# Kernel optimization log

Hardware: AMD Instinct MI355X
Metric: run time of the kernel (lower is better)

The kernel has to match this reference:

```python
import jax, jax.numpy as jnp
import numpy as np

NUM_GROUPS = 64  # matches fill_max of ids; all groups present w.h.p. so unique-inverse == ids


def setup_inputs() -> dict:
    key = jax.random.key(0)
    ks = jax.random.split(key, 8)
    B, N, D = 8, 8192, 512
    s = 1.0 / np.sqrt(D)
    return {
        "x": jax.random.normal(ks[0], (B, N, D), dtype=jnp.float32),
        "ids": jax.random.randint(ks[1], (N,), 0, NUM_GROUPS),
        "w1": jax.random.normal(ks[2], (D, D), dtype=jnp.float32) * s,
        "b1": jax.random.normal(ks[3], (D,), dtype=jnp.float32) * s,
        "w2": jax.random.normal(ks[4], (D, D), dtype=jnp.float32) * s,
        "b2": jax.random.normal(ks[5], (D,), dtype=jnp.float32) * s,
        "w3": jax.random.normal(ks[6], (D, D), dtype=jnp.float32) * s,
        "b3": jax.random.normal(ks[7], (D,), dtype=jnp.float32) * s,
    }


def reference(x, ids, w1, b1, w2, b2, w3, b3):
    # x: [B, N, D]; ids: [N] group labels in [0, NUM_GROUPS)
    G = NUM_GROUPS
    a = jnp.einsum('bnd,ed->bne', x, w1) + b1          # linear1 logits
    v = jnp.einsum('bnd,ed->bne', x, w2) + b2          # linear2 values
    # move segment axis to front: [N, B, D]
    aT = jnp.transpose(a, (1, 0, 2))
    vT = jnp.transpose(v, (1, 0, 2))
    # per-group stable softmax along the segment axis
    mx = jax.lax.stop_gradient(jax.ops.segment_max(aT, ids, num_segments=G))  # [G,B,D]
    ex = jnp.exp(aT - mx[ids])
    denom = jax.ops.segment_sum(ex, ids, num_segments=G)                      # [G,B,D]
    wts = ex / denom[ids]                                                     # [N,B,D]
    # weighted scatter-sum of values -> [G, B, D] -> [B, G, D]
    y = jnp.transpose(jax.ops.segment_sum(vT * wts, ids, num_segments=G), (1, 0, 2))
    out = jnp.einsum('bgd,ed->bge', y, w3) + b3        # linear3
    # expand: gather group outputs back to per-element rows -> [B, N, D]
    return out[:, ids]
```

## Files before the change

kernel.cpp:

```cpp
#include <hip/hip_runtime.h>
#include <hip/hip_bf16.h>
#include <math.h>

#define B_ 8
#define N_ 8192
#define D_ 512
#define G_ 64
#define M_ (B_ * N_)

typedef short bf16x8 __attribute__((ext_vector_type(8)));
typedef float f32x4 __attribute__((ext_vector_type(4)));

__device__ __forceinline__ unsigned short f2bf(float f) {
    __hip_bfloat16 h = __float2bfloat16(f);
    return *reinterpret_cast<unsigned short*>(&h);
}
__device__ __forceinline__ void gload_lds16(const void* g, void* l) {
    __builtin_amdgcn_global_load_lds((const __attribute__((address_space(1))) void*)g,
                                     (__attribute__((address_space(3))) void*)l,
                                     16, 0, 0);
}

__global__ __launch_bounds__(256) void cast_xp(const float* __restrict__ x,
                                               const int* __restrict__ perm,
                                               unsigned short* __restrict__ xb) {
    const int total = M_ * 128;
    for (int idx = blockIdx.x * 256 + threadIdx.x; idx < total;
         idx += gridDim.x * 256) {
        const int row = idx >> 7;
        const int q = (idx & 127) * 4;
        const int b = row >> 13;
        const int i = row & 8191;
        const float* src = x + (((size_t)(b << 13) + perm[i]) << 9) + q;
        float4 f = *(const float4*)src;
        ushort4 u;
        u.x = f2bf(f.x); u.y = f2bf(f.y); u.z = f2bf(f.z); u.w = f2bf(f.w);
        *(ushort4*)(xb + ((size_t)row << 9) + q) = u;
    }
}

__global__ __launch_bounds__(256) void cast_w(const float* __restrict__ w1,
                                              const float* __restrict__ b1,
                                              const float* __restrict__ w2,
                                              const float* __restrict__ b2,
                                              unsigned short* __restrict__ wB,
                                              float* __restrict__ biasB) {
    int t = blockIdx.x * 256 + threadIdx.x;
    int idx = t * 4;
    int row = idx >> 9;
    int col = idx & 511;
    const float* src = (row < 512) ? (w1 + (size_t)row * 512 + col)
                                   : (w2 + (size_t)(row - 512) * 512 + col);
    float4 f = *(const float4*)src;
    ushort4 u;
    u.x = f2bf(f.x); u.y = f2bf(f.y); u.z = f2bf(f.z); u.w = f2bf(f.w);
    *(ushort4*)(wB + idx) = u;
    if (t < 1024) biasB[t] = (t < 512) ? b1[t] : b2[t - 512];
}

__global__ __launch_bounds__(256) void bl_hist(const int* __restrict__ ids,
                                               int* __restrict__ counts,
                                               int* __restrict__ stripbase) {
    __shared__ int sid[N_];
    __shared__ int sc[256];
    const int g = blockIdx.x;
    const int t = threadIdx.x;
    for (int i = t; i < N_; i += 256) sid[i] = ids[i];
    __syncthreads();
    int c = 0;
    const int nb = t * 32;
#pragma unroll 8
    for (int k = 0; k < 32; ++k) c += (sid[nb + k] == g) ? 1 : 0;
    sc[t] = c;
    __syncthreads();
    if (t == 0) {
        int run = 0;
        for (int i = 0; i < 256; ++i) { int v = sc[i]; sc[i] = run; run += v; }
        counts[g] = run;
    }
    __syncthreads();
    stripbase[g * 256 + t] = sc[t];
}

__global__ __launch_bounds__(256) void bl_emit(const int* __restrict__ ids,
                                               const int* __restrict__ counts,
                                               const int* __restrict__ stripbase,
                                               int* __restrict__ baseO,
                                               int* __restrict__ fgO,
                                               int* __restrict__ perm) {
    __shared__ int sid[N_];
    __shared__ int sb[G_ + 1];
    __shared__ int sbs;
    const int g = blockIdx.x;
    const int t = threadIdx.x;
    for (int i = t; i < N_; i += 256) sid[i] = ids[i];
    if (t == 0) {
        int a = 0;
        for (int gg = 0; gg < G_; ++gg) { sb[gg] = a; a += counts[gg]; }
        sb[G_] = a;
        sbs = sb[g];
    }
    __syncthreads();
    if (g == 0 && t < G_) {
        baseO[t] = sb[t];
        const int row = t * 128;
        int gg = 0;
        while (gg + 1 < G_ && sb[gg + 1] <= row) ++gg;
        fgO[t] = gg;
    }
    int pos = sbs + stripbase[g * 256 + t];
    const int nb = t * 32;
    for (int k = 0; k < 32; ++k)
        if (sid[nb + k] == g) perm[pos++] = nb + k;
}

__global__ __launch_bounds__(512, 2) void gemm_fused(const unsigned short* __restrict__ xb,
                                                     const unsigned short* __restrict__ wB,
                                                     const float* __restrict__ biasB,
                                                     const int* __restrict__ base,
                                                     const int* __restrict__ fg,
                                                     float* __restrict__ pt) {
    extern __shared__ unsigned short smem[];
    unsigned short* lsA = smem;
    unsigned short* lsB = smem + 32768;

    const int o  = blockIdx.x;
    const int mt = (o & 7) + ((o >> 5) << 3);
    const int nt = (o >> 3) & 3;
    const int b  = mt >> 5;
    const int tlb = (mt & 31) * 2;
    const int c0 = nt * 128;

    const int tid = threadIdx.x;
    const int l = tid & 63;
    const int w = tid >> 6;
    const int wm = w >> 2;
    const int wn = w & 3;
    const int lr = l >> 3;
    const int lslot = l & 7;
    const int fr = l & 15;
    const int kq = l >> 4;
    const int scol = 8 * (lslot ^ lr);

    f32x4 acc[8][4];
#pragma unroll
    for (int i = 0; i < 8; ++i)
#pragma unroll
        for (int j = 0; j < 4; ++j) acc[i][j] = (f32x4){0.f, 0.f, 0.f, 0.f};

    const size_t abase = (((size_t)b << 13) + (size_t)(mt & 31) * 256) << 9;

    auto stage8 = [&](int slot, int kt) {
#pragma unroll
        for (int q = 0; q < 4; ++q) {
            const int c = w * 4 + q;
            const int row = c * 8 + lr;
            gload_lds16(xb + abase + ((size_t)row << 9) + kt + scol,
                        lsA + slot * 16384 + c * 512);
        }
#pragma unroll
        for (int q = 0; q < 4; ++q) {
            const int c = w * 4 + q;
            const int srcrow = ((c >> 2) & 1) * 512 + c0 + (c >> 3) * 32
                             + (c & 3) * 8 + lr;
            gload_lds16(wB + ((size_t)srcrow << 9) + kt + scol,
                        lsB + slot * 16384 + c * 512);
        }
    };

    stage8(0, 0);
    stage8(1, 64);

    for (int i4 = 0; i4 < 4; ++i4) {
#pragma unroll
        for (int half = 0; half < 2; ++half) {
            const int slot = half;
            const bool doStage = (half == 0) ? (i4 > 0) : (i4 < 3);
            if (doStage) stage8(1 - half, (2 * i4 + 1 + half) * 64);
            if (doStage || (half == 0)) {
                asm volatile("s_waitcnt vmcnt(8)" ::: "memory");
            } else {
                asm volatile("s_waitcnt vmcnt(0)" ::: "memory");
            }
            __builtin_amdgcn_s_barrier();

            const unsigned short* pA = lsA + slot * 16384;
            const unsigned short* pB = lsB + slot * 16384;
            bf16x8 bq[4];
#pragma unroll
            for (int ks = 0; ks < 2; ++ks) {
                const int ib = 8 * ((ks * 4 + kq) ^ (fr & 7));
#pragma unroll
                for (int ih = 0; ih < 2; ++ih) {
                    bf16x8 a[4];
#pragma unroll
                    for (int i = 0; i < 4; ++i)
                        a[i] = *(const bf16x8*)&pA[(wm * 128 + (ih * 4 + i) * 16 + fr) * 64 + ib];
                    if (ih == 0) {
#pragma unroll
                        for (int j = 0; j < 4; ++j)
                            bq[j] = *(const bf16x8*)&pB[(wn * 64 + j * 16 + fr) * 64 + ib];
                    }
                    __builtin_amdgcn_s_barrier();
                    __builtin_amdgcn_s_setprio(1);
#pragma unroll
                    for (int i = 0; i < 4; ++i)
#pragma unroll
                        for (int j = 0; j < 4; ++j)
                            acc[ih * 4 + i][j] = __builtin_amdgcn_mfma_f32_16x16x32_bf16(
                                a[i], bq[j], acc[ih * 4 + i][j], 0, 0, 0);
                    __builtin_amdgcn_s_setprio(0);
                    __builtin_amdgcn_s_barrier();
                }
            }
        }
    }

    const int tl = tlb + wm;
    const int fg0 = fg[tl];
    const int bnd0 = (fg0 + 1 < G_) ? base[fg0 + 1] : (1 << 30);
    const int bnd1 = (fg0 + 2 < G_) ? base[fg0 + 2] : (1 << 30);
    const int bnd2 = (fg0 + 3 < G_) ? base[fg0 + 3] : (1 << 30);
    float b1c[2], b2c[2];
#pragma unroll
    for (int j = 0; j < 2; ++j) {
        const int col = c0 + wn * 32 + j * 16 + fr;
        b1c[j] = biasB[col];
        b2c[j] = biasB[512 + col];
    }
    float dp[4][2] = {}, yp[4][2] = {};
    const int rbase = tl * 128 + kq * 4;
#pragma unroll
    for (int i = 0; i < 8; ++i)
#pragma unroll
        for (int rr = 0; rr < 4; ++rr) {
            const int row = rbase + i * 16 + rr;
            const int s = (row >= bnd0) + (row >= bnd1) + (row >= bnd2);
#pragma unroll
            for (int j = 0; j < 2; ++j) {
                const float e = __expf(acc[i][j][rr] + b1c[j]);
                const float ey = e * (acc[i][j + 2][rr] + b2c[j]);
#pragma unroll
                for (int s2 = 0; s2 < 4; ++s2) {
                    dp[s2][j] += (s == s2) ? e : 0.f;
                    yp[s2][j] += (s == s2) ? ey : 0.f;
                }
            }
        }
#pragma unroll
    for (int s2 = 0; s2 < 4; ++s2)
#pragma unroll
        for (int j = 0; j < 2; ++j) {
            dp[s2][j] += __shfl_xor(dp[s2][j], 16);
            dp[s2][j] += __shfl_xor(dp[s2][j], 32);
            yp[s2][j] += __shfl_xor(yp[s2][j], 16);
            yp[s2][j] += __shfl_xor(yp[s2][j], 32);
        }
    if (kq == 0) {
#pragma unroll
        for (int s2 = 0; s2 < 4; ++s2)
#pragma unroll
            for (int j = 0; j < 2; ++j) {
                const int colp = c0 + wn * 32 + j * 16 + fr;
                float2 v = make_float2(dp[s2][j], yp[s2][j]);
                *(float2*)&pt[(((size_t)(b * 64 + tl) * 4 + s2) * 512 + colp) * 2] = v;
            }
    }
}

__global__ __launch_bounds__(256) void combineC(const float* __restrict__ pt,
                                                const int* __restrict__ base,
                                                const int* __restrict__ counts,
                                                const int* __restrict__ fg,
                                                float* __restrict__ y) {
    const int g = blockIdx.x, b = blockIdx.y;
    const int bs = base[g];
    int cnt = counts[g];
    if (cnt == 0) cnt = 1;
    const int t0 = bs >> 7, t1 = (bs + cnt - 1) >> 7;
    for (int c = threadIdx.x; c < 512; c += 256) {
        float d = 0.f, yy = 0.f;
        for (int t = t0; t <= t1; ++t) {
            const int s = g - fg[t];
            if (s >= 0 && s < 4) {
                const float* p = &pt[((((size_t)(b * 64 + t)) * 4 + s) * 512 + c) * 2];
                d += p[0];
                yy += p[1];
            }
        }
        y[((size_t)(b * G_ + g)) * 512 + c] = yy / d;
    }
}

__global__ __launch_bounds__(256) void gemm3(const float* __restrict__ y,
                                             const float* __restrict__ w3,
                                             const float* __restrict__ b3,
                                             float* __restrict__ out_small) {
    __shared__ float ys[16][68];
    __shared__ float wss[16][68];
    const int m0 = blockIdx.x * 64;
    const int n0 = blockIdx.y * 64;
    const int tid = threadIdx.x;
    const int tr = tid >> 4;
    const int tc = tid & 15;
    const int lrow = tid >> 2;
    const int lk4 = (tid & 3) * 4;

    float acc[4][4] = {};

    for (int k0 = 0; k0 < D_; k0 += 16) {
        float4 yv = *(const float4*)(y + (size_t)(m0 + lrow) * D_ + k0 + lk4);
        float4 wv = *(const float4*)(w3 + (size_t)(n0 + lrow) * D_ + k0 + lk4);
        __syncthreads();
        ys[lk4 + 0][lrow] = yv.x;  ys[lk4 + 1][lrow] = yv.y;
        ys[lk4 + 2][lrow] = yv.z;  ys[lk4 + 3][lrow] = yv.w;
        wss[lk4 + 0][lrow] = wv.x; wss[lk4 + 1][lrow] = wv.y;
        wss[lk4 + 2][lrow] = wv.z; wss[lk4 + 3][lrow] = wv.w;
        __syncthreads();
#pragma unroll
        for (int kk = 0; kk < 16; ++kk) {
            float4 y4 = *(const float4*)&ys[kk][tr * 4];
            float4 w4 = *(const float4*)&wss[kk][tc * 4];
            float ya[4] = {y4.x, y4.y, y4.z, y4.w};
            float wa[4] = {w4.x, w4.y, w4.z, w4.w};
#pragma unroll
            for (int i = 0; i < 4; ++i)
#pragma unroll
                for (int j = 0; j < 4; ++j)
                    acc[i][j] = fmaf(ya[i], wa[j], acc[i][j]);
        }
    }

    float bb[4];
#pragma unroll
    for (int j = 0; j < 4; ++j) bb[j] = b3[n0 + tc * 4 + j];
#pragma unroll
    for (int i = 0; i < 4; ++i) {
        size_t o = (size_t)(m0 + tr * 4 + i) * D_ + n0 + tc * 4;
        float4 r;
        r.x = acc[i][0] + bb[0]; r.y = acc[i][1] + bb[1];
        r.z = acc[i][2] + bb[2]; r.w = acc[i][3] + bb[3];
        *(float4*)(out_small + o) = r;
    }
}

__global__ __launch_bounds__(256) void gather_out(const int* __restrict__ ids,
                                                  const float* __restrict__ out_small,
                                                  float* __restrict__ out) {
    const int c = blockIdx.x * 256 + threadIdx.x;
    const int per_row = D_ / 4;
    const int b = c / (N_ * per_row);
    const int rem = c % (N_ * per_row);
    const int n = rem / per_row;
    const int q = rem % per_row;
    const int g = ids[n];
    float4 val = *(const float4*)(out_small + ((size_t)b * G_ + g) * D_ + q * 4);
    *(float4*)(out + (size_t)c * 4) = val;
}

extern "C" void kernel_launch(void* const* d_in, const int* in_sizes, int n_in,
                              void* d_out, int out_size, void* d_ws, size_t ws_size,
                              hipStream_t stream) {
    (void)in_sizes; (void)n_in; (void)out_size; (void)ws_size;
    const float* x   = (const float*)d_in[0];
    const int*   ids = (const int*)d_in[1];
    const float* w1  = (const float*)d_in[2];
    const float* b1  = (const float*)d_in[3];
    const float* w2  = (const float*)d_in[4];
    const float* b2  = (const float*)d_in[5];
    const float* w3  = (const float*)d_in[6];
    const float* b3  = (const float*)d_in[7];
    float* out = (float*)d_out;

    float* ws_f = (float*)d_ws;
    unsigned short* xb = (unsigned short*)ws_f;
    float* after_xb  = ws_f + 16777216;
    unsigned short* wB = (unsigned short*)after_xb;
    float* biasB     = after_xb + 262144;
    float* pt        = biasB + 1024;
    float* y         = pt + 2097152;
    float* out_small = y + 262144;
    int*   perm      = (int*)(out_small + 262144);
    int*   base      = perm + N_;
    int*   counts    = base + G_;
    int*   fg        = counts + G_;
    int*   stripbase = fg + G_;

    hipFuncSetAttribute((const void*)gemm_fused,
                        hipFuncAttributeMaxDynamicSharedMemorySize, 131072);

    hipLaunchKernelGGL(bl_hist, dim3(G_), dim3(256), 0, stream, ids, counts, stripbase);
    hipLaunchKernelGGL(bl_emit, dim3(G_), dim3(256), 0, stream,
                       ids, counts, stripbase, base, fg, perm);
    hipLaunchKernelGGL(cast_w, dim3(512), dim3(256), 0, stream, w1, b1, w2, b2, wB, biasB);
    hipLaunchKernelGGL(cast_xp, dim3(2048), dim3(256), 0, stream, x, perm, xb);
    hipLaunchKernelGGL(gemm_fused, dim3(1024), dim3(512), 131072, stream,
                       xb, wB, biasB, base, fg, pt);
    hipLaunchKernelGGL(combineC, dim3(G_, B_), dim3(256), 0, stream, pt, base, counts, fg, y);
    hipLaunchKernelGGL(gemm3, dim3(8, 8), dim3(256), 0, stream, y, w3, b3, out_small);
    hipLaunchKernelGGL(gather_out, dim3(32768), dim3(256), 0, stream, ids, out_small, out);
}
```

Before: 204.6 us.

## Interleave next-tile global-to-LDS prefetch across MFMA phases in GEMM main loop

```diff
diff --git a/kernel.cpp b/kernel.cpp
--- a/kernel.cpp
+++ b/kernel.cpp
@@ -150,68 +150,66 @@
 
     const size_t abase = (((size_t)b << 13) + (size_t)(mt & 31) * 256) << 9;
 
-    auto stage8 = [&](int slot, int kt) {
-#pragma unroll
-        for (int q = 0; q < 4; ++q) {
-            const int c = w * 4 + q;
-            const int row = c * 8 + lr;
-            gload_lds16(xb + abase + ((size_t)row << 9) + kt + scol,
-                        lsA + slot * 16384 + c * 512);
-        }
-#pragma unroll
-        for (int q = 0; q < 4; ++q) {
-            const int c = w * 4 + q;
-            const int srcrow = ((c >> 2) & 1) * 512 + c0 + (c >> 3) * 32
-                             + (c & 3) * 8 + lr;
-            gload_lds16(wB + ((size_t)srcrow << 9) + kt + scol,
-                        lsB + slot * 16384 + c * 512);
-        }
+    auto stageA = [&](int slot, int kt, int q) {
+        const int c = w * 4 + q;
+        const int row = c * 8 + lr;
+        gload_lds16(xb + abase + ((size_t)row << 9) + kt + scol,
+                    lsA + slot * 16384 + c * 512);
     };
-
-    stage8(0, 0);
-    stage8(1, 64);
-
-    for (int i4 = 0; i4 < 4; ++i4) {
-#pragma unroll
-        for (int half = 0; half < 2; ++half) {
-            const int slot = half;
-            const bool doStage = (half == 0) ? (i4 > 0) : (i4 < 3);
-            if (doStage) stage8(1 - half, (2 * i4 + 1 + half) * 64);
-            if (doStage || (half == 0)) {
-                asm volatile("s_waitcnt vmcnt(8)" ::: "memory");
-            } else {
-                asm volatile("s_waitcnt vmcnt(0)" ::: "memory");
-            }
-            __builtin_amdgcn_s_barrier();
-
-            const unsigned short* pA = lsA + slot * 16384;
-            const unsigned short* pB = lsB + slot * 16384;
-            bf16x8 bq[4];
-#pragma unroll
-            for (int ks = 0; ks < 2; ++ks) {
-                const int ib = 8 * ((ks * 4 + kq) ^ (fr & 7));
-#pragma unroll
-                for (int ih = 0; ih < 2; ++ih) {
-                    bf16x8 a[4];
-#pragma unroll
-                    for (int i = 0; i < 4; ++i)
-                        a[i] = *(const bf16x8*)&pA[(wm * 128 + (ih * 4 + i) * 16 + fr) * 64 + ib];
-                    if (ih == 0) {
-#pragma unroll
-                        for (int j = 0; j < 4; ++j)
-                            bq[j] = *(const bf16x8*)&pB[(wn * 64 + j * 16 + fr) * 64 + ib];
-                    }
-                    __builtin_amdgcn_s_barrier();
-                    __builtin_amdgcn_s_setprio(1);
-#pragma unroll
-                    for (int i = 0; i < 4; ++i)
-#pragma unroll
-                        for (int j = 0; j < 4; ++j)
-                            acc[ih * 4 + i][j] = __builtin_amdgcn_mfma_f32_16x16x32_bf16(
-                                a[i], bq[j], acc[ih * 4 + i][j], 0, 0, 0);
-                    __builtin_amdgcn_s_setprio(0);
-                    __builtin_amdgcn_s_barrier();
+    auto stageB = [&](int slot, int kt, int q) {
+        const int c = w * 4 + q;
+        const int srcrow = ((c >> 2) & 1) * 512 + c0 + (c >> 3) * 32
+                         + (c & 3) * 8 + lr;
+        gload_lds16(wB + ((size_t)srcrow << 9) + kt + scol,
+                    lsB + slot * 16384 + c * 512);
+    };
+
+#pragma unroll
+    for (int q = 0; q < 4; ++q) stageA(0, 0, q);
+#pragma unroll
+    for (int q = 0; q < 4; ++q) stageB(0, 0, q);
+    asm volatile("s_waitcnt vmcnt(0)" ::: "memory");
+    __builtin_amdgcn_s_barrier();
+
+    for (int t = 0; t < 8; ++t) {
+        const int slot = t & 1;
+        const int so = slot ^ 1;
+        const int kn = (t + 1) * 64;
+        const bool pf = (t < 7);
+        const unsigned short* pA = lsA + slot * 16384;
+        const unsigned short* pB = lsB + slot * 16384;
+        bf16x8 a[4], bq[4];
+
+#pragma unroll
+        for (int ks = 0; ks < 2; ++ks) {
+            const int ib = 8 * ((ks * 4 + kq) ^ (fr & 7));
+#pragma unroll
+            for (int ih = 0; ih < 2; ++ih) {
+                if (pf) {
+                    if (ks == 0 && ih == 0) { stageA(so, kn, 0); stageA(so, kn, 1); stageB(so, kn, 0); }
+                    else if (ks == 0 && ih == 1) { stageA(so, kn, 2); stageA(so, kn, 3); stageB(so, kn, 1); }
+                    else if (ks == 1 && ih == 0) { stageB(so, kn, 2); stageB(so, kn, 3); }
                 }
+#pragma unroll
+                for (int i = 0; i < 4; ++i)
+                    a[i] = *(const bf16x8*)&pA[(wm * 128 + (ih * 4 + i) * 16 + fr) * 64 + ib];
+                if (ih == 0) {
+#pragma unroll
+                    for (int j = 0; j < 4; ++j)
+                        bq[j] = *(const bf16x8*)&pB[(wn * 64 + j * 16 + fr) * 64 + ib];
+                }
+                __builtin_amdgcn_s_barrier();
+                __builtin_amdgcn_s_setprio(1);
+#pragma unroll
+                for (int i = 0; i < 4; ++i)
+#pragma unroll
+                    for (int j = 0; j < 4; ++j)
+                        acc[ih * 4 + i][j] = __builtin_amdgcn_mfma_f32_16x16x32_bf16(
+                            a[i], bq[j], acc[ih * 4 + i][j], 0, 0, 0);
+                __builtin_amdgcn_s_setprio(0);
+                if (ks == 1 && ih == 1)
+                    asm volatile("s_waitcnt vmcnt(0)" ::: "memory");
+                __builtin_amdgcn_s_barrier();
             }
         }
     }
```

Measured after the change: 202.4 us. No clear change (-1.1%).
